# Kernel tuning notes

Measured on AMD Instinct MI355X. Metric: run time of the kernel, lower is better.

## Reference

```python
import jax, jax.numpy as jnp
import numpy as np
import math

T_SCALE = 99
FEAT_DIM = 400
BATCH = 2
C = 256
NH = 8
NS = 32
NSPB = 3
RATIO = 0.5
LOCAL_STEP = 33


def build_sample_mask(T=T_SCALE, ns=NS, nspb=NSPB, ratio=RATIO):
    # Vectorized port of _get_interp1d_mask. Flat layout: [time, (bin, start, end)].
    N = ns * nspb
    e_idx, s_idx = np.meshgrid(np.arange(T), np.arange(T), indexing='ij')
    valid = s_idx < e_idx
    starts_i = s_idx[valid].astype(np.int64)
    ends_i = e_idx[valid].astype(np.int64)
    starts = starts_i.astype(np.float64)
    ends = ends_i.astype(np.float64)
    center = ends - starts + 1.0
    xmin = starts - center * ratio
    plen = (ends + center * ratio) - xmin
    S = xmin[:, None] + (plen / (N - 1.0))[:, None] * np.arange(N)[None, :]  # [P, N]
    down = np.trunc(S).astype(np.int64)  # matches int(math.modf(s)[1]) (trunc toward 0)
    dec = S - down                       # can be negative when s < 0, as in the original
    up = np.ceil(S).astype(np.int64)
    bin_col = (np.arange(N) // nspb)[None, :] * (T * T) + (starts_i * T + ends_i)[:, None]
    M = np.zeros(T * ns * T * T, np.float64)
    vd = (down >= 0) & (down <= T - 1)
    np.add.at(M, (down * (ns * T * T) + bin_col)[vd], ((1.0 - dec) / nspb)[vd])
    vu = (up >= 0) & (up <= T - 1)
    np.add.at(M, (up * (ns * T * T) + bin_col)[vu], (dec / nspb)[vu])
    return M.reshape(T, ns * T * T).astype(np.float32)


def pos_ebb(scale, size):
    pos = jnp.arange(scale, dtype=jnp.float32)[:, None]
    div = jnp.exp(jnp.arange(0, size, 2, dtype=jnp.float32) * (-math.log(10000.0) / size))
    ang = pos * div
    # interleave sin (even) / cos (odd)
    return jnp.stack([jnp.sin(ang), jnp.cos(ang)], axis=-1).reshape(scale, size)


def layer_norm(x, g, b, eps=1e-5):
    mu = jnp.mean(x, -1, keepdims=True)
    var = jnp.mean((x - mu) ** 2, -1, keepdims=True)
    return (x - mu) * jax.lax.rsqrt(var + eps) * g + b


def mha(x, w_qkv, b_qkv, w_o, b_o, nh=NH):
    t, b, c = x.shape
    hd = c // nh
    q, k, v = jnp.split(x @ w_qkv.T + b_qkv, 3, axis=-1)
    q = q.reshape(t, b, nh, hd)
    k = k.reshape(t, b, nh, hd)
    v = v.reshape(t, b, nh, hd)
    att = jnp.einsum('qbhd,kbhd->bhqk', q, k) / math.sqrt(hd)
    att = jax.nn.softmax(att, axis=-1)
    o = jnp.einsum('bhqk,kbhd->qbhd', att, v).reshape(t, b, c)
    return o @ w_o.T + b_o


def encoder(x, p):
    # PyTorch post-norm TransformerEncoder (eval mode, dropout off) + final LayerNorm
    (qkv_w, qkv_b, o_w, o_b, l1_w, l1_b, l2_w, l2_b, n1_g, n1_b, n2_g, n2_b, nf_g, nf_b) = p
    for i in range(qkv_w.shape[0]):
        a = mha(x, qkv_w[i], qkv_b[i], o_w[i], o_b[i])
        x = layer_norm(x + a, n1_g[i], n1_b[i])
        f = jax.nn.relu(x @ l1_w[i].T + l1_b[i]) @ l2_w[i].T + l2_b[i]
        x = layer_norm(x + f, n2_g[i], n2_b[i])
    return layer_norm(x, nf_g, nf_b)


def conv1d(x, w, b, pad, groups=1):
    y = jax.lax.conv_general_dilated(x, w, (1,), [(pad, pad)],
                                     dimension_numbers=('NCH', 'OIH', 'NCH'),
                                     feature_group_count=groups)
    return y + b[None, :, None]


def conv2d(x, w, b, pad):
    y = jax.lax.conv_general_dilated(x, w, (1, 1), [(pad, pad), (pad, pad)],
                                     dimension_numbers=('NCHW', 'OIHW', 'NCHW'))
    return y + b[None, :, None, None]


def conv3d(x, w, b, stride):
    y = jax.lax.conv_general_dilated(x, w, stride, [(0, 0)] * 3,
                                     dimension_numbers=('NCDHW', 'OIDHW', 'NCDHW'))
    return y + b[None, :, None, None, None]


def _forward(x, cb_w, cb_b, tg_qkv_w, tg_qkv_b, tg_o_w, tg_o_b, tg_l1_w, tg_l1_b, tg_l2_w, tg_l2_b, tg_n1_g, tg_n1_b, tg_n2_g, tg_n2_b, tg_nf_g, tg_nf_b, tl_qkv_w, tl_qkv_b, tl_o_w, tl_o_b, tl_l1_w, tl_l1_b, tl_l2_w, tl_l2_b, tl_n1_g, tl_n1_b, tl_n2_g, tl_n2_b, tl_nf_g, tl_nf_b, s1_w, s1_b, s2_w, s2_b, c3_w, c3_b, p1_w, p1_b, p2_w, p2_b, p3_w, p3_b, sample_mask):
    B, _, T = x.shape
    base = jax.nn.relu(conv1d(x, cb_w, cb_b, pad=1, groups=4))  # [B,C,T]
    # local transformer on LOCAL_STEP-strided windows
    group = T // LOCAL_STEP
    tl_p = (tl_qkv_w, tl_qkv_b, tl_o_w, tl_o_b, tl_l1_w, tl_l1_b, tl_l2_w, tl_l2_b, tl_n1_g, tl_n1_b, tl_n2_g, tl_n2_b, tl_nf_g, tl_nf_b)
    feat = base.reshape(B, C, LOCAL_STEP, group).transpose(2, 3, 0, 1).reshape(LOCAL_STEP, B * group, C)
    feat = encoder(feat + pos_ebb(LOCAL_STEP, C)[:, None, :], tl_p)
    local = feat.reshape(LOCAL_STEP * group, B, C).transpose(1, 2, 0)  # [B,C,T]
    # global bidirectional transformer (shared weights, flipped second pass)
    tg_p = (tg_qkv_w, tg_qkv_b, tg_o_w, tg_o_b, tg_l1_w, tg_l1_b, tg_l2_w, tg_l2_b, tg_n1_g, tg_n1_b, tg_n2_g, tg_n2_b, tg_nf_g, tg_nf_b)
    g = base.transpose(2, 0, 1)  # [T,B,C]
    pe = pos_ebb(T, C)[:, None, :]
    f1 = encoder(g + pe, tg_p)
    f2 = encoder(g[::-1] + pe, tg_p)
    base2 = local + (f1 + f2[::-1]).transpose(1, 2, 0)  # [B,C,T]
    s = jax.nn.relu(conv1d(base2, s1_w, s1_b, pad=1, groups=4))
    start1 = jax.nn.sigmoid(conv1d(s, s2_w, s2_b, pad=0))[:, 0, :]  # [B,T]
    # boundary-matching layer: dense matmul against precomputed interp mask
    bm = jnp.matmul(base2, sample_mask).reshape(B, C, NS, T, T)
    p = jax.nn.relu(conv3d(bm, c3_w, c3_b, (NS, 1, 1)))[:, :, 0]  # [B,C,T,T]
    p = jax.nn.relu(conv2d(p, p1_w, p1_b, pad=1))
    p = jax.nn.relu(conv2d(p, p2_w, p2_b, pad=1))
    cm = jax.nn.sigmoid(conv2d(p, p3_w, p3_b, pad=0))  # [B,2,T,T]
    return cm, start1


def setup_inputs() -> dict:
    key = jax.random.key(0)
    ks = iter(jax.random.split(key, 80))
    def rnd(shape):
        return 0.02 * jax.random.normal(next(ks), shape, dtype=jnp.float32)
    inp = {'x': jax.random.normal(next(ks), (BATCH, FEAT_DIM, T_SCALE), dtype=jnp.float32)}
    inp['cb_w'] = rnd((C, FEAT_DIM // 4, 3)); inp['cb_b'] = jnp.zeros((C,), jnp.float32)
    for pre, n in (('tg', 6), ('tl', 3)):
        inp[pre + '_qkv_w'] = rnd((n, 3 * C, C)); inp[pre + '_qkv_b'] = jnp.zeros((n, 3 * C), jnp.float32)
        inp[pre + '_o_w'] = rnd((n, C, C)); inp[pre + '_o_b'] = jnp.zeros((n, C), jnp.float32)
        inp[pre + '_l1_w'] = rnd((n, 1024, C)); inp[pre + '_l1_b'] = jnp.zeros((n, 1024), jnp.float32)
        inp[pre + '_l2_w'] = rnd((n, C, 1024)); inp[pre + '_l2_b'] = jnp.zeros((n, C), jnp.float32)
        inp[pre + '_n1_g'] = jnp.ones((n, C), jnp.float32); inp[pre + '_n1_b'] = jnp.zeros((n, C), jnp.float32)
        inp[pre + '_n2_g'] = jnp.ones((n, C), jnp.float32); inp[pre + '_n2_b'] = jnp.zeros((n, C), jnp.float32)
        inp[pre + '_nf_g'] = jnp.ones((C,), jnp.float32); inp[pre + '_nf_b'] = jnp.zeros((C,), jnp.float32)
    inp['s1_w'] = rnd((C, C // 4, 3)); inp['s1_b'] = jnp.zeros((C,), jnp.float32)
    inp['s2_w'] = rnd((1, C, 1)); inp['s2_b'] = jnp.zeros((1,), jnp.float32)
    inp['c3_w'] = rnd((C, C, NS, 1, 1)); inp['c3_b'] = jnp.zeros((C,), jnp.float32)
    inp['p1_w'] = rnd((C, C, 3, 3)); inp['p1_b'] = jnp.zeros((C,), jnp.float32)
    inp['p2_w'] = rnd((C, C, 3, 3)); inp['p2_b'] = jnp.zeros((C,), jnp.float32)
    inp['p3_w'] = rnd((2, C, 1, 1)); inp['p3_b'] = jnp.zeros((2,), jnp.float32)
    inp['sample_mask'] = jnp.asarray(build_sample_mask())  # [T, NS*T*T], exact BMN interp mask
    return inp


def reference(x, cb_w, cb_b, tg_qkv_w, tg_qkv_b, tg_o_w, tg_o_b, tg_l1_w, tg_l1_b, tg_l2_w, tg_l2_b, tg_n1_g, tg_n1_b, tg_n2_g, tg_n2_b, tg_nf_g, tg_nf_b, tl_qkv_w, tl_qkv_b, tl_o_w, tl_o_b, tl_l1_w, tl_l1_b, tl_l2_w, tl_l2_b, tl_n1_g, tl_n1_b, tl_n2_g, tl_n2_b, tl_nf_g, tl_nf_b, s1_w, s1_b, s2_w, s2_b, c3_w, c3_b, p1_w, p1_b, p2_w, p2_b, p3_w, p3_b, sample_mask):
    return _forward(x, cb_w, cb_b, tg_qkv_w, tg_qkv_b, tg_o_w, tg_o_b, tg_l1_w, tg_l1_b, tg_l2_w, tg_l2_b, tg_n1_g, tg_n1_b, tg_n2_g, tg_n2_b, tg_nf_g, tg_nf_b, tl_qkv_w, tl_qkv_b, tl_o_w, tl_o_b, tl_l1_w, tl_l1_b, tl_l2_w, tl_l2_b, tl_n1_g, tl_n1_b, tl_n2_g, tl_n2_b, tl_nf_g, tl_nf_b, s1_w, s1_b, s2_w, s2_b, c3_w, c3_b, p1_w, p1_b, p2_w, p2_b, p3_w, p3_b, sample_mask)
```

## Files before the change

### kernel.cpp

```cpp
#include <hip/hip_runtime.h>
#include <math.h>

#define T99   99
#define CC    256
#define NHH   8
#define FEAT  400
#define NS_   32
#define LSTEP 33

typedef __attribute__((ext_vector_type(8))) short s8v;
typedef __attribute__((ext_vector_type(4))) float f4v;

__device__ __forceinline__ void mfma_bf16(f4v& d, s8v a, s8v b) {
  asm("v_mfma_f32_16x16x32_bf16 %0, %1, %2, %0" : "+v"(d) : "v"(a), "v"(b));
}

__device__ __forceinline__ unsigned short f2bf(float f) {
  union { float f; unsigned u; } x; x.f = f;
  unsigned r = x.u + 0x7FFFu + ((x.u >> 16) & 1u);
  return (unsigned short)(r >> 16);
}
__device__ __forceinline__ float bf2f(unsigned short h) {
  union { unsigned u; float f; } x; x.u = ((unsigned)h) << 16;
  return x.f;
}
__device__ __forceinline__ float blo(unsigned u) { union { unsigned x; float f; } c; c.x = u << 16; return c.f; }
__device__ __forceinline__ float bhi(unsigned u) { union { unsigned x; float f; } c; c.x = u & 0xffff0000u; return c.f; }

__device__ __forceinline__ float pe_val(int pos, int c) {
  int i = c >> 1;
  float freq = expf((float)(2 * i) * (-0.03597789207803197f));
  float ang = (float)pos * freq;
  return (c & 1) ? cosf(ang) : sinf(ang);
}

__global__ __launch_bounds__(128) void k_convbase(const float* __restrict__ x,
                                                  const float* __restrict__ w,
                                                  const float* __restrict__ bias,
                                                  float* __restrict__ base) {
  int b = blockIdx.x >> 8, co = blockIdx.x & 255, t = threadIdx.x;
  if (t >= T99) return;
  int g = co >> 6;
  float acc = bias[co];
  const float* xp = x + (size_t)(b * FEAT + g * 100) * T99;
  const float* wp = w + (size_t)co * 300;
  for (int ic = 0; ic < 100; ++ic) {
    float x0 = (t > 0)  ? xp[ic * T99 + t - 1] : 0.f;
    float x1 = xp[ic * T99 + t];
    float x2 = (t < 98) ? xp[ic * T99 + t + 1] : 0.f;
    acc += wp[ic * 3] * x0 + wp[ic * 3 + 1] * x1 + wp[ic * 3 + 2] * x2;
  }
  base[(size_t)(b * CC + co) * T99 + t] = fmaxf(acc, 0.f);
}

__global__ __launch_bounds__(256) void k_convW(const float* __restrict__ qkv, const float* __restrict__ o,
                                               const float* __restrict__ l1, const float* __restrict__ l2,
                                               int L, unsigned short* __restrict__ dst) {
  int total = L * 786432;
  for (int idx = blockIdx.x * 256 + threadIdx.x; idx < total; idx += gridDim.x * 256) {
    int l = idx / 786432, r = idx % 786432;
    float v;
    if (r < 196608)      v = qkv[(size_t)l * 196608 + r];
    else if (r < 262144) v = o[(size_t)l * 65536 + (r - 196608)];
    else if (r < 524288) v = l1[(size_t)l * 262144 + (r - 262144)];
    else                 v = l2[(size_t)l * 262144 + (r - 524288)];
    dst[idx] = f2bf(v);
  }
}

__global__ __launch_bounds__(256) void k_build_xg(const float* __restrict__ base, float* __restrict__ xg,
                                                  unsigned short* __restrict__ xgb) {
  int idx = blockIdx.x * 256 + threadIdx.x;
  int t = idx >> 10, r = idx & 1023, b4 = r >> 8, c = r & 255;
  float v = (b4 < 2) ? base[(size_t)(b4 * CC + c) * T99 + t]
                     : base[(size_t)((b4 - 2) * CC + c) * T99 + (98 - t)];
  v += pe_val(t, c);
  xg[idx] = v; xgb[idx] = f2bf(v);
}

__global__ __launch_bounds__(256) void k_build_xl(const float* __restrict__ base, float* __restrict__ xl,
                                                  unsigned short* __restrict__ xlb) {
  int idx = blockIdx.x * 256 + threadIdx.x;
  int ls = idx / 1536, r = idx % 1536, j = r >> 8, c = r & 255;
  int g = j >> 1, b = j & 1, t = ls * 3 + g;
  float v = base[(size_t)(b * CC + c) * T99 + t] + pe_val(ls, c);
  xl[idx] = v; xlb[idx] = f2bf(v);
}

struct GJ {
  const unsigned short* Ab;
  const unsigned short* W;
  const float* bias;
  const float* R;
  float* Yf;
  unsigned short* Yb;
  int M, N, K, flags;
};

__device__ void g_body(const GJ& j, int m0, int n0) {
  __shared__ __align__(16) unsigned short Al[64][264];
  __shared__ __align__(16) unsigned short Bl[64][264];
  int tid = threadIdx.x, lane = tid & 63, w = tid >> 6, wm = w >> 1, wn = w & 1;
  f4v acc[2][2];
#pragma unroll
  for (int mt = 0; mt < 2; ++mt)
#pragma unroll
    for (int nt = 0; nt < 2; ++nt) acc[mt][nt] = (f4v){0.f, 0.f, 0.f, 0.f};

  for (int kc0 = 0; kc0 < j.K; kc0 += 256) {
#pragma unroll
    for (int it = 0; it < 8; ++it) {
      int idx = it * 256 + tid, row = idx >> 5, seg = (idx & 31) << 3;
      s8v av = {0, 0, 0, 0, 0, 0, 0, 0};
      if (m0 + row < j.M) av = *(const s8v*)&j.Ab[(size_t)(m0 + row) * j.K + kc0 + seg];
      *(s8v*)&Al[row][seg] = av;
      *(s8v*)&Bl[row][seg] = *(const s8v*)&j.W[(size_t)(n0 + row) * j.K + kc0 + seg];
    }
    __syncthreads();
#pragma unroll
    for (int kst = 0; kst < 8; ++kst) {
      int kcol = kst * 32 + (lane >> 4) * 8;
      s8v af[2], bf[2];
#pragma unroll
      for (int mt = 0; mt < 2; ++mt)
        af[mt] = *(const s8v*)&Al[wm * 32 + mt * 16 + (lane & 15)][kcol];
#pragma unroll
      for (int nt = 0; nt < 2; ++nt)
        bf[nt] = *(const s8v*)&Bl[wn * 32 + nt * 16 + (lane & 15)][kcol];
#pragma unroll
      for (int mt = 0; mt < 2; ++mt)
#pragma unroll
        for (int nt = 0; nt < 2; ++nt) mfma_bf16(acc[mt][nt], af[mt], bf[nt]);
    }
    __syncthreads();
  }
  asm volatile("s_nop 7\n\ts_nop 7\n\ts_nop 4");
#pragma unroll
  for (int mt = 0; mt < 2; ++mt) {
#pragma unroll
    for (int nt = 0; nt < 2; ++nt) {
      int col = n0 + wn * 32 + nt * 16 + (lane & 15);
      float bv = j.bias[col];
#pragma unroll
      for (int r = 0; r < 4; ++r) {
        int row = m0 + wm * 32 + mt * 16 + (lane >> 4) * 4 + r;
        if (row < j.M) {
          float v = acc[mt][nt][r] + bv;
          if (j.flags & 2) v += j.R[(size_t)row * j.N + col];
          if (j.flags & 1) v = fmaxf(v, 0.f);
          if (!(j.flags & 8)) j.Yf[(size_t)row * j.N + col] = v;
          if (j.flags & 4) j.Yb[(size_t)row * j.N + col] = f2bf(v);
        }
      }
    }
  }
}

__global__ __launch_bounds__(256) void k_g(GJ j) {
  if ((int)blockIdx.x * 64 >= j.M) return;
  g_body(j, blockIdx.x * 64, blockIdx.y * 64);
}

__global__ __launch_bounds__(256) void k_g2(GJ j0, GJ j1) {
  if (blockIdx.z == 0) {
    if ((int)blockIdx.x * 64 >= j0.M) return;
    g_body(j0, blockIdx.x * 64, blockIdx.y * 64);
  } else {
    if ((int)blockIdx.x * 64 >= j1.M) return;
    g_body(j1, blockIdx.x * 64, blockIdx.y * 64);
  }
}

__device__ __forceinline__ void attn_body(const unsigned short* __restrict__ qkv,
                                          unsigned short* __restrict__ attb,
                                          int T_, int B_, int bid) {
  __shared__ float qv[32];
  __shared__ float red[128];
  __shared__ float pv[128];
  int tid = threadIdx.x;
  int q = bid % T_;
  int h = (bid / T_) % NHH;
  int b = bid / (T_ * NHH);
  if (tid < 32) qv[tid] = bf2f(qkv[(size_t)(q * B_ + b) * 768 + h * 32 + tid]);
  __syncthreads();
  float s = -1e30f;
  if (tid < T_) {
    const unsigned short* kp = qkv + (size_t)(tid * B_ + b) * 768 + 256 + h * 32;
    float d = 0;
#pragma unroll
    for (int i = 0; i < 32; ++i) d += qv[i] * bf2f(kp[i]);
    s = d * 0.176776695296636881f;
  }
  red[tid] = s; __syncthreads();
  for (int o = 64; o > 0; o >>= 1) { if (tid < o) red[tid] = fmaxf(red[tid], red[tid + o]); __syncthreads(); }
  float mx = red[0]; __syncthreads();
  float p = (tid < T_) ? expf(s - mx) : 0.f;
  pv[tid] = p; red[tid] = p; __syncthreads();
  for (int o = 64; o > 0; o >>= 1) { if (tid < o) red[tid] += red[tid + o]; __syncthreads(); }
  float denom = red[0];
  __syncthreads();
  int d = tid & 31, part = tid >> 5;
  float o = 0.f;
  for (int k = part; k < T_; k += 4)
    o += pv[k] * bf2f(qkv[(size_t)(k * B_ + b) * 768 + 512 + h * 32 + d]);
  red[tid] = o; __syncthreads();
  if (tid < 32) {
    float t = red[tid] + red[tid + 32] + red[tid + 64] + red[tid + 96];
    attb[(size_t)(q * B_ + b) * 256 + h * 32 + tid] = f2bf(t / denom);
  }
}

__global__ __launch_bounds__(128) void k_attn(const unsigned short* __restrict__ qkv,
                                              unsigned short* __restrict__ attb, int T_, int B_) {
  attn_body(qkv, attb, T_, B_, blockIdx.x);
}

__global__ __launch_bounds__(128) void k_attn2(const unsigned short* __restrict__ qkv0,
                                               unsigned short* __restrict__ attb0, int T0, int B0,
                                               const unsigned short* __restrict__ qkv1,
                                               unsigned short* __restrict__ attb1, int T1, int B1) {
  int bid = blockIdx.x;
  if (blockIdx.z == 0) {
    if (bid >= B0 * NHH * T0) return;
    attn_body(qkv0, attb0, T0, B0, bid);
  } else {
    if (bid >= B1 * NHH * T1) return;
    attn_body(qkv1, attb1, T1, B1, bid);
  }
}

__device__ __forceinline__ void ln_body(const float* __restrict__ X, const float* __restrict__ g,
                                        const float* __restrict__ bb, float* __restrict__ Y,
                                        unsigned short* __restrict__ Yb, int tok) {
  __shared__ float rs[256], rq[256];
  int c = threadIdx.x;
  float v = X[(size_t)tok * 256 + c];
  rs[c] = v; rq[c] = v * v; __syncthreads();
  for (int o = 128; o > 0; o >>= 1) { if (c < o) { rs[c] += rs[c + o]; rq[c] += rq[c + o]; } __syncthreads(); }
  float mu = rs[0] * (1.f / 256.f);
  float var = rq[0] * (1.f / 256.f) - mu * mu;
  float r = (v - mu) * rsqrtf(var + 1e-5f) * g[c] + bb[c];
  Y[(size_t)tok * 256 + c] = r;
  if (Yb) Yb[(size_t)tok * 256 + c] = f2bf(r);
}

__global__ __launch_bounds__(256) void k_ln(const float* __restrict__ X, const float* __restrict__ g,
                                            const float* __restrict__ bb, float* __restrict__ Y,
                                            unsigned short* __restrict__ Yb) {
  ln_body(X, g, bb, Y, Yb, blockIdx.x);
}

__global__ __launch_bounds__(256) void k_ln2(const float* __restrict__ X0, const float* __restrict__ g0,
                                             const float* __restrict__ bb0, float* __restrict__ Y0,
                                             unsigned short* __restrict__ Yb0, int n0,
                                             const float* __restrict__ X1, const float* __restrict__ g1,
                                             const float* __restrict__ bb1, float* __restrict__ Y1,
                                             unsigned short* __restrict__ Yb1, int n1) {
  int tok = blockIdx.x;
  if (blockIdx.z == 0) { if (tok < n0) ln_body(X0, g0, bb0, Y0, Yb0, tok); }
  else                 { if (tok < n1) ln_body(X1, g1, bb1, Y1, Yb1, tok); }
}

__global__ __launch_bounds__(256) void k_combine(const float* __restrict__ encl, const float* __restrict__ encg,
                                                 float* __restrict__ base2) {
  int idx = blockIdx.x * 256 + threadIdx.x;
  int t = idx % T99, c = (idx / T99) & 255, b = idx / (CC * T99);
  int ls = t / 3, g = t % 3;
  float v = encl[(size_t)(ls * 6 + g * 2 + b) * 256 + c]
          + encg[(size_t)(t * 4 + b) * 256 + c]
          + encg[(size_t)((98 - t) * 4 + 2 + b) * 256 + c];
  base2[idx] = v;
}

__global__ __launch_bounds__(256) void k_sfuse(const float* __restrict__ base2, const float* __restrict__ s1w,
                                               const float* __restrict__ s1b, const float* __restrict__ s2w,
                                               const float* __restrict__ s2b, float* __restrict__ out) {
  __shared__ float rs[256];
  int b = blockIdx.x / T99, t = blockIdx.x % T99, co = threadIdx.x;
  int g = co >> 6;
  float acc = s1b[co];
  const float* xp = base2 + (size_t)(b * CC + g * 64) * T99;
  const float* wp = s1w + (size_t)co * 192;
  for (int ic = 0; ic < 64; ++ic) {
    float x0 = (t > 0)  ? xp[ic * T99 + t - 1] : 0.f;
    float x1 = xp[ic * T99 + t];
    float x2 = (t < 98) ? xp[ic * T99 + t + 1] : 0.f;
    acc += wp[ic * 3] * x0 + wp[ic * 3 + 1] * x1 + wp[ic * 3 + 2] * x2;
  }
  rs[co] = fmaxf(acc, 0.f) * s2w[co];
  __syncthreads();
  for (int o = 128; o > 0; o >>= 1) { if (co < o) rs[co] += rs[co + o]; __syncthreads(); }
  if (co == 0) out[blockIdx.x] = 1.f / (1.f + expf(-(rs[0] + s2b[0])));
}

__global__ __launch_bounds__(256) void k_w3t(const float* __restrict__ c3w, float* __restrict__ w3t) {
  int idx = blockIdx.x * 256 + threadIdx.x;
  int co = idx & 255, ci = (idx >> 8) & 255, n = idx >> 16;
  w3t[idx] = c3w[((size_t)(co << 8) + ci) * 32 + n];
}

__global__ __launch_bounds__(256) void k_G(const float* __restrict__ w3t, const float* __restrict__ base2,
                                           unsigned short* __restrict__ Gb) {
  int tc = blockIdx.x, n = blockIdx.y, b = blockIdx.z;
  int co = threadIdx.x;
  int t0 = tc * 25;
  float acc[25];
#pragma unroll
  for (int q = 0; q < 25; ++q) acc[q] = 0.f;
  const float* w = w3t + (size_t)n * 65536 + co;
  const float* bs = base2 + (size_t)b * CC * T99 + t0;
  for (int ci = 0; ci < 256; ++ci) {
    float wv = w[(size_t)ci * 256];
#pragma unroll
    for (int q = 0; q < 25; ++q) acc[q] += wv * bs[ci * T99 + q];
  }
#pragma unroll
  for (int q = 0; q < 25; ++q) {
    int t = t0 + q;
    if (t < T99) Gb[((size_t)(n * T99 + t) * 256 + co) * 2 + b] = f2bf(acc[q]);
  }
  if (tc == 0 && n == 0 && b == 0)
    ((unsigned int*)(Gb + (size_t)NS_ * T99 * 512))[co] = 0u;
}

__global__ __launch_bounds__(256) void k_ppre(const unsigned short* __restrict__ Gb,
                                              const float* __restrict__ c3b,
                                              unsigned int* __restrict__ pinb32) {
  __shared__ float w0s[96], w1s[96];
  __shared__ int   ofs[96];
  __shared__ float part[128][4];
  int e = blockIdx.x % T99, s = blockIdx.x / T99;
  int tid = threadIdx.x;
  if (s >= e) {
    if (tid < 128) {
      float z0 = fmaxf(c3b[2 * tid], 0.f), z1 = fmaxf(c3b[2 * tid + 1], 0.f);
      unsigned int zz = ((unsigned)f2bf(z1) << 16) | (unsigned)f2bf(z0);
      pinb32[((size_t)s * T99 + e) * 128 + tid] = zz;
      pinb32[((size_t)(T99 + s) * T99 + e) * 128 + tid] = zz;
    }
    return;
  }
  if (tid < 96) {
    double center = (double)(e - s + 1);
    double S = ((double)s - 0.5 * center) + ((2.0 * center - 1.0) / 95.0) * (double)tid;
    double dn = trunc(S);
    double dec = S - dn;
    int di = (int)dn;
    double uc = ceil(S);
    int ui = (int)uc;
    int n = tid / 3;
    float w0 = 0.f, w1 = 0.f;
    int r0 = 0;
    if (dn >= 0.0 && dn <= 98.0) {
      r0 = di;
      w0 = (float)((1.0 - dec) / 3.0);
      if (uc >= 0.0 && uc <= 98.0) {
        if (ui == di) w0 += (float)(dec / 3.0);
        else          w1  = (float)(dec / 3.0);
      }
    }
    w0s[tid] = w0; w1s[tid] = w1;
    ofs[tid] = (n * T99 + r0) * 1024;
  }
  __syncthreads();
  int ch = tid & 127, half = tid >> 7;
  float a00 = 0.f, a01 = 0.f, a10 = 0.f, a11 = 0.f;
  const char* basep = (const char*)Gb + ch * 8;
  int k0 = half * 48;
#pragma unroll 8
  for (int k = k0; k < k0 + 48; ++k) {
    float w0 = w0s[k], w1 = w1s[k];
    const uint2* p = (const uint2*)(basep + ofs[k]);
    uint2 u0 = p[0];
    uint2 u1 = p[128];
    a00 += w0 * blo(u0.x) + w1 * blo(u1.x);
    a01 += w0 * bhi(u0.x) + w1 * bhi(u1.x);
    a10 += w0 * blo(u0.y) + w1 * blo(u1.y);
    a11 += w0 * bhi(u0.y) + w1 * bhi(u1.y);
  }
  if (half) { part[ch][0] = a00; part[ch][1] = a01; part[ch][2] = a10; part[ch][3] = a11; }
  __syncthreads();
  if (tid < 128) {
    a00 += part[ch][0]; a01 += part[ch][1]; a10 += part[ch][2]; a11 += part[ch][3];
    float b0 = c3b[2 * tid], b1 = c3b[2 * tid + 1];
    unsigned int zb0 = ((unsigned)f2bf(fmaxf(a10 + b1, 0.f)) << 16) | (unsigned)f2bf(fmaxf(a00 + b0, 0.f));
    unsigned int zb1 = ((unsigned)f2bf(fmaxf(a11 + b1, 0.f)) << 16) | (unsigned)f2bf(fmaxf(a01 + b0, 0.f));
    pinb32[((size_t)s * T99 + e) * 128 + tid] = zb0;
    pinb32[((size_t)(T99 + s) * T99 + e) * 128 + tid] = zb1;
  }
}

__global__ __launch_bounds__(256) void k_wb2(const float* __restrict__ pw, unsigned short* __restrict__ wbf) {
  int idx = blockIdx.x * 256 + threadIdx.x;
  if (idx >= 73728) return;
  int lane = idx & 63;
  int cog  = (idx >> 6) & 15;
  int kst  = (idx >> 10) & 7;
  int tap  = idx >> 13;
  int co = cog * 16 + (lane & 15);
  int k  = kst * 32 + (lane >> 4) * 8;
  s8v v;
#pragma unroll
  for (int j = 0; j < 8; ++j)
    v[j] = (short)f2bf(pw[((size_t)co * 256 + k + j) * 9 + tap]);
  *(s8v*)&wbf[(size_t)idx * 8] = v;
}

__global__ __launch_bounds__(256) void k_cvec(const float* __restrict__ pw, const float* __restrict__ cin,
                                              const float* __restrict__ bias, int reluCin,
                                              float* __restrict__ coutF, unsigned short* __restrict__ coutB) {
  __shared__ float rs[256];
  int co = blockIdx.x, ci = threadIdx.x;
  float c = cin[ci];
  if (reluCin) c = fmaxf(c, 0.f);
  const float* wp = pw + ((size_t)co * 256 + ci) * 9;
  float wsum = 0.f;
#pragma unroll
  for (int t = 0; t < 9; ++t) wsum += wp[t];
  rs[ci] = wsum * c;
  __syncthreads();
  for (int o = 128; o > 0; o >>= 1) { if (ci < o) rs[ci] += rs[ci + o]; __syncthreads(); }
  if (ci == 0) {
    float r = fmaxf(bias[co] + rs[0], 0.f);
    coutF[co] = r;
    coutB[co] = f2bf(r);
  }
}

__device__ __forceinline__ int aoff(int s) {
  int tap = s >> 3, kst = s & 7;
  return ((tap / 3) * 10 + (tap % 3)) * 264 + kst * 32;
}
__device__ __forceinline__ void ldb4(const unsigned short* __restrict__ B0, int s, s8v* dst) {
#pragma unroll
  for (int nt = 0; nt < 4; ++nt) dst[nt] = *(const s8v*)(B0 + (size_t)s * 8192 + nt * 512);
}

__global__ __launch_bounds__(256) void k_conv3x3(const unsigned short* __restrict__ in,
                                                 const unsigned short* __restrict__ wbf,
                                                 const float* __restrict__ bias,
                                                 const unsigned short* __restrict__ cvecB,
                                                 int D, int lo, int hi,
                                                 unsigned short* __restrict__ out) {
  __shared__ __align__(16) unsigned short Ah[100 * 264];
  int b = blockIdx.z;
  int co0 = blockIdx.y * 128;
  int ti = blockIdx.x / 13, tj = blockIdx.x % 13;
  int i0 = ti * 8, j0 = tj * 8;
  int tid = threadIdx.x;

  if (i0 - 1 >= lo && i0 + 8 <= hi && j0 - 1 >= lo && j0 + 8 <= hi && i0 - 1 >= j0 + 8 + D) {
    const unsigned int* cv = (const unsigned int*)(cvecB + co0);
    unsigned int* ob = (unsigned int*)out;
#pragma unroll
    for (int r = 0; r < 16; ++r) {
      int idx = r * 256 + tid;
      int sp = idx >> 6, cp = idx & 63;
      int gi = i0 + (sp >> 3), gj = j0 + (sp & 7);
      ob[((size_t)(b * T99 + gi) * T99 + gj) * 128 + (co0 >> 1) + cp] = cv[cp];
    }
    return;
  }

#pragma unroll
  for (int it = 0; it < 13; ++it) {
    int chunk = it * 256 + tid;
    if (chunk < 3200) {
      int row = chunk >> 5;
      int cc = (chunk & 31) * 8;
      int gi = i0 + row / 10 - 1, gj = j0 + row % 10 - 1;
      s8v val = {0, 0, 0, 0, 0, 0, 0, 0};
      if (gi >= 0 && gi < T99 && gj >= 0 && gj < T99)
        val = *(const s8v*)&in[((size_t)(b * T99 + gi) * T99 + gj) * 256 + cc];
      *(s8v*)&Ah[row * 264 + cc] = val;
    }
  }
  __syncthreads();

  int lane = tid & 63, w = tid >> 6, wm = w >> 1, wn = w & 1;
  int l15 = lane & 15, lk = lane >> 4;
  int spL0 = wm * 32 + l15, spL1 = spL0 + 16;
  int hr0 = (spL0 >> 3) * 10 + (spL0 & 7);
  int hr1 = (spL1 >> 3) * 10 + (spL1 & 7);
  const unsigned short* A0 = &Ah[hr0 * 264 + lk * 8];
  const unsigned short* A1 = &Ah[hr1 * 264 + lk * 8];
  int cogbase = blockIdx.y * 8 + wn * 4;
  const unsigned short* B0 = wbf + (size_t)cogbase * 512 + (size_t)lane * 8;

  f4v acc[2][4];
#pragma unroll
  for (int mt = 0; mt < 2; ++mt)
#pragma unroll
    for (int nt = 0; nt < 4; ++nt) acc[mt][nt] = (f4v){0.f, 0.f, 0.f, 0.f};

  s8v a0c, a1c, a0n, a1n;
  s8v bq[3][4];
  a0c = *(const s8v*)(A0 + aoff(0));
  a1c = *(const s8v*)(A1 + aoff(0));
  a0n = a0c; a1n = a1c;
  ldb4(B0, 0, bq[0]);
  ldb4(B0, 1, bq[1]);
#pragma unroll
  for (int s = 0; s < 72; ++s) {
    if (s + 2 < 72) ldb4(B0, s + 2, bq[(s + 2) % 3]);
    if (s + 1 < 72) {
      a0n = *(const s8v*)(A0 + aoff(s + 1));
      a1n = *(const s8v*)(A1 + aoff(s + 1));
    }
#pragma unroll
    for (int nt = 0; nt < 4; ++nt) {
      mfma_bf16(acc[0][nt], a0c, bq[s % 3][nt]);
      mfma_bf16(acc[1][nt], a1c, bq[s % 3][nt]);
    }
    a0c = a0n; a1c = a1n;
  }

  asm volatile("s_nop 7\n\ts_nop 7\n\ts_nop 4");
#pragma unroll
  for (int mt = 0; mt < 2; ++mt) {
#pragma unroll
    for (int nt = 0; nt < 4; ++nt) {
      int co = co0 + wn * 64 + nt * 16 + l15;
      float bv = bias[co];
#pragma unroll
      for (int r = 0; r < 4; ++r) {
        int sp = wm * 32 + mt * 16 + lk * 4 + r;
        int gi = i0 + (sp >> 3), gj = j0 + (sp & 7);
        if (gi < T99 && gj < T99) {
          float v = fmaxf(acc[mt][nt][r] + bv, 0.f);
          out[((size_t)(b * T99 + gi) * T99 + gj) * 256 + co] = f2bf(v);
        }
      }
    }
  }
}

__global__ __launch_bounds__(256) void k_p3(const unsigned short* __restrict__ p2o,
                                            const float* __restrict__ w, const float* __restrict__ bias,
                                            float* __restrict__ cm) {
  int idx = blockIdx.x * 256 + threadIdx.x;
  if (idx >= 2 * T99 * T99) return;
  int j = idx % T99, i = (idx / T99) % T99, b = idx / (T99 * T99);
  float a0 = bias[0], a1 = bias[1];
  const unsigned short* row = p2o + ((size_t)(b * T99 + i) * T99 + j) * 256;
  for (int c8 = 0; c8 < 256; c8 += 8) {
    s8v v = *(const s8v*)&row[c8];
#pragma unroll
    for (int q = 0; q < 8; ++q) {
      float x = bf2f((unsigned short)v[q]);
      a0 += w[c8 + q] * x;
      a1 += w[256 + c8 + q] * x;
    }
  }
  size_t base = (size_t)b * 2 * T99 * T99 + (size_t)i * T99 + j;
  cm[base] = 1.f / (1.f + expf(-a0));
  cm[base + T99 * T99] = 1.f / (1.f + expf(-a1));
}

struct EncW {
  const float *qkvw, *qkvb, *ow, *ob, *l1w, *l1b, *l2w, *l2b, *n1g, *n1b, *n2g, *n2b, *nfg, *nfb;
};
struct EncBufs {
  float* x; unsigned short* xb;
  float* yb;
  unsigned short *qkvb, *attb, *hb;
  int M;
};

static GJ jqkv(const EncW& W, const unsigned short* Wb, int l, const EncBufs& B) {
  GJ j = {}; j.Ab = B.xb; j.W = Wb + (size_t)l * 786432;
  j.bias = W.qkvb + (size_t)l * 768; j.Yb = B.qkvb; j.flags = 4 | 8;
  j.M = B.M; j.N = 768; j.K = 256; return j;
}
static GJ jproj(const EncW& W, const unsigned short* Wb, int l, const EncBufs& B) {
  GJ j = {}; j.Ab = B.attb; j.W = Wb + (size_t)l * 786432 + 196608;
  j.bias = W.ob + (size_t)l * 256; j.R = B.x; j.Yf = B.yb; j.flags = 2;
  j.M = B.M; j.N = 256; j.K = 256; return j;
}
static GJ jffn1(const EncW& W, const unsigned short* Wb, int l, const EncBufs& B) {
  GJ j = {}; j.Ab = B.xb; j.W = Wb + (size_t)l * 786432 + 262144;
  j.bias = W.l1b + (size_t)l * 1024; j.Yb = B.hb; j.flags = 1 | 4 | 8;
  j.M = B.M; j.N = 1024; j.K = 256; return j;
}
static GJ jffn2(const EncW& W, const unsigned short* Wb, int l, const EncBufs& B) {
  GJ j = {}; j.Ab = B.hb; j.W = Wb + (size_t)l * 786432 + 524288;
  j.bias = W.l2b + (size_t)l * 256; j.R = B.x; j.Yf = B.yb; j.flags = 2;
  j.M = B.M; j.N = 256; j.K = 1024; return j;
}

extern "C" void kernel_launch(void* const* d_in, const int* in_sizes, int n_in,
                              void* d_out, int out_size, void* d_ws, size_t ws_size,
                              hipStream_t stream) {
  (void)in_sizes; (void)n_in; (void)out_size; (void)ws_size;
  const float* x    = (const float*)d_in[0];
  const float* cbw  = (const float*)d_in[1];
  const float* cbb  = (const float*)d_in[2];
  EncW tg = {(const float*)d_in[3],  (const float*)d_in[4],  (const float*)d_in[5],  (const float*)d_in[6],
             (const float*)d_in[7],  (const float*)d_in[8],  (const float*)d_in[9],  (const float*)d_in[10],
             (const float*)d_in[11], (const float*)d_in[12], (const float*)d_in[13], (const float*)d_in[14],
             (const float*)d_in[15], (const float*)d_in[16]};
  EncW tl = {(const float*)d_in[17], (const float*)d_in[18], (const float*)d_in[19], (const float*)d_in[20],
             (const float*)d_in[21], (const float*)d_in[22], (const float*)d_in[23], (const float*)d_in[24],
             (const float*)d_in[25], (const float*)d_in[26], (const float*)d_in[27], (const float*)d_in[28],
             (const float*)d_in[29], (const float*)d_in[30]};
  const float* s1w = (const float*)d_in[31];
  const float* s1b = (const float*)d_in[32];
  const float* s2w = (const float*)d_in[33];
  const float* s2b = (const float*)d_in[34];
  const float* c3w = (const float*)d_in[35];
  const float* c3b = (const float*)d_in[36];
  const float* p1w = (const float*)d_in[37];
  const float* p1b = (const float*)d_in[38];
  const float* p2w = (const float*)d_in[39];
  const float* p2b = (const float*)d_in[40];
  const float* p3w = (const float*)d_in[41];
  const float* p3b = (const float*)d_in[42];

  float* outp = (float*)d_out;

  char* wp = (char*)d_ws;
  auto alloc = [&](size_t bytes) -> void* {
    void* p = (void*)wp;
    wp += (bytes + 255) & ~(size_t)255;
    return p;
  };
  float* base  = (float*)alloc(sizeof(float) * 2 * CC * T99);
  const int ML = 198, MG = 396;
  EncBufs BG, BL;
  BG.M = MG; BL.M = ML;
  BG.x  = (float*)alloc(sizeof(float) * MG * 256);
  BL.x  = (float*)alloc(sizeof(float) * ML * 256);
  BG.xb = (unsigned short*)alloc(sizeof(short) * MG * 256);
  BL.xb = (unsigned short*)alloc(sizeof(short) * ML * 256);
  BG.yb = (float*)alloc(sizeof(float) * MG * 256);
  BL.yb = (float*)alloc(sizeof(float) * ML * 256);
  BG.qkvb = (unsigned short*)alloc(sizeof(short) * MG * 768);
  BL.qkvb = (unsigned short*)alloc(sizeof(short) * ML * 768);
  BG.attb = (unsigned short*)alloc(sizeof(short) * MG * 256);
  BL.attb = (unsigned short*)alloc(sizeof(short) * ML * 256);
  BG.hb = (unsigned short*)alloc(sizeof(short) * MG * 1024);
  BL.hb = (unsigned short*)alloc(sizeof(short) * ML * 1024);
  float* encg  = (float*)alloc(sizeof(float) * MG * 256);
  float* encl  = (float*)alloc(sizeof(float) * ML * 256);
  float* base2 = (float*)alloc(sizeof(float) * 2 * CC * T99);
  float* w3t   = (float*)alloc(sizeof(float) * 32 * 256 * 256);
  unsigned short* Gb = (unsigned short*)alloc(sizeof(short) * (2 * NS_ * T99 * 256 + 512));
  unsigned short* pinb = (unsigned short*)alloc(sizeof(short) * 2 * T99 * T99 * 256);
  unsigned short* p1o  = (unsigned short*)alloc(sizeof(short) * 2 * T99 * T99 * 256);
  unsigned short* p2o  = (unsigned short*)alloc(sizeof(short) * 2 * T99 * T99 * 256);
  unsigned short* wb2a = (unsigned short*)alloc(sizeof(short) * 9 * 256 * 256);
  unsigned short* wb2b = (unsigned short*)alloc(sizeof(short) * 9 * 256 * 256);
  unsigned short* wtgb = (unsigned short*)alloc(sizeof(short) * 6 * 786432);
  unsigned short* wtlb = (unsigned short*)alloc(sizeof(short) * 3 * 786432);
  float* c1F = (float*)alloc(sizeof(float) * 256);
  unsigned short* c1B = (unsigned short*)alloc(sizeof(short) * 256);
  float* c2F = (float*)alloc(sizeof(float) * 256);
  unsigned short* c2B = (unsigned short*)alloc(sizeof(short) * 256);

  k_convW<<<dim3(4096), dim3(256), 0, stream>>>(tg.qkvw, tg.ow, tg.l1w, tg.l2w, 6, wtgb);
  k_convW<<<dim3(2048), dim3(256), 0, stream>>>(tl.qkvw, tl.ow, tl.l1w, tl.l2w, 3, wtlb);
  k_w3t<<<dim3(8192), dim3(256), 0, stream>>>(c3w, w3t);
  k_wb2<<<dim3(288), dim3(256), 0, stream>>>(p1w, wb2a);
  k_wb2<<<dim3(288), dim3(256), 0, stream>>>(p2w, wb2b);
  k_cvec<<<dim3(256), dim3(256), 0, stream>>>(p1w, c3b, p1b, 1, c1F, c1B);
  k_cvec<<<dim3(256), dim3(256), 0, stream>>>(p2w, c1F, p2b, 0, c2F, c2B);
  k_convbase<<<dim3(512), dim3(128), 0, stream>>>(x, cbw, cbb, base);
  k_build_xl<<<dim3(198), dim3(256), 0, stream>>>(base, BL.x, BL.xb);
  k_build_xg<<<dim3(396), dim3(256), 0, stream>>>(base, BG.x, BG.xb);

  const int mgG = 7;
  for (int l = 0; l < 3; ++l) {
    k_g2<<<dim3(mgG, 12, 2), dim3(256), 0, stream>>>(jqkv(tl, wtlb, l, BL), jqkv(tg, wtgb, l, BG));
    k_attn2<<<dim3(4 * NHH * T99, 1, 2), dim3(128), 0, stream>>>(BL.qkvb, BL.attb, LSTEP, 6,
                                                                 BG.qkvb, BG.attb, T99, 4);
    k_g2<<<dim3(mgG, 4, 2), dim3(256), 0, stream>>>(jproj(tl, wtlb, l, BL), jproj(tg, wtgb, l, BG));
    k_ln2<<<dim3(MG, 1, 2), dim3(256), 0, stream>>>(BL.yb, tl.n1g + l * 256, tl.n1b + l * 256, BL.x, BL.xb, ML,
                                                    BG.yb, tg.n1g + l * 256, tg.n1b + l * 256, BG.x, BG.xb, MG);
    k_g2<<<dim3(mgG, 16, 2), dim3(256), 0, stream>>>(jffn1(tl, wtlb, l, BL), jffn1(tg, wtgb, l, BG));
    k_g2<<<dim3(mgG, 4, 2), dim3(256), 0, stream>>>(jffn2(tl, wtlb, l, BL), jffn2(tg, wtgb, l, BG));
    k_ln2<<<dim3(MG, 1, 2), dim3(256), 0, stream>>>(BL.yb, tl.n2g + l * 256, tl.n2b + l * 256, BL.x, BL.xb, ML,
                                                    BG.yb, tg.n2g + l * 256, tg.n2b + l * 256, BG.x, BG.xb, MG);
  }
  for (int l = 3; l < 6; ++l) {
    k_g<<<dim3(mgG, 12), dim3(256), 0, stream>>>(jqkv(tg, wtgb, l, BG));
    k_attn<<<dim3(4 * NHH * T99), dim3(128), 0, stream>>>(BG.qkvb, BG.attb, T99, 4);
    k_g<<<dim3(mgG, 4), dim3(256), 0, stream>>>(jproj(tg, wtgb, l, BG));
    k_ln<<<dim3(MG), dim3(256), 0, stream>>>(BG.yb, tg.n1g + l * 256, tg.n1b + l * 256, BG.x, BG.xb);
    k_g<<<dim3(mgG, 16), dim3(256), 0, stream>>>(jffn1(tg, wtgb, l, BG));
    k_g<<<dim3(mgG, 4), dim3(256), 0, stream>>>(jffn2(tg, wtgb, l, BG));
    k_ln<<<dim3(MG), dim3(256), 0, stream>>>(BG.yb, tg.n2g + l * 256, tg.n2b + l * 256, BG.x, BG.xb);
  }
  k_ln2<<<dim3(MG, 1, 2), dim3(256), 0, stream>>>(BL.x, tl.nfg, tl.nfb, encl, nullptr, ML,
                                                  BG.x, tg.nfg, tg.nfb, encg, nullptr, MG);
  k_combine<<<dim3(198), dim3(256), 0, stream>>>(encl, encg, base2);
  k_sfuse<<<dim3(198), dim3(256), 0, stream>>>(base2, s1w, s1b, s2w, s2b, outp + 2 * 2 * T99 * T99);
  k_G<<<dim3(4, 32, 2), dim3(256), 0, stream>>>(w3t, base2, Gb);
  k_ppre<<<dim3(T99 * T99), dim3(256), 0, stream>>>(Gb, c3b, (unsigned int*)pinb);
  k_conv3x3<<<dim3(169, 2, 2), dim3(256), 0, stream>>>(pinb, wb2a, p1b, c1B, 0, 0, 98, p1o);
  k_conv3x3<<<dim3(169, 2, 2), dim3(256), 0, stream>>>(p1o, wb2b, p2b, c2B, 2, 1, 97, p2o);
  k_p3<<<dim3(77), dim3(256), 0, stream>>>(p2o, p3w, p3b, outp);
}
```

Before: 688.1 us.

## Move G projection to bf16 MFMA and shrink GEMM LDS tiles to K=32

The fp32 scalar k_G kernel becomes an MFMA-based bf16 GEMM (k_Gm). It uses a transposed bf16 copy of base2 produced in k_combine and a bf16 transposed weight w3tb. The shared transformer GEMM body also now stages 32-wide K slices instead of 256-wide ones. This shrinks LDS use, which should allow higher occupancy, but adds more barriers per K step. Rounding the G inputs to bf16 lowers precision.

```diff
diff --git a/kernel.cpp b/kernel.cpp
--- a/kernel.cpp
+++ b/kernel.cpp
@@ -98,40 +98,35 @@
 };
 
 __device__ void g_body(const GJ& j, int m0, int n0) {
-  __shared__ __align__(16) unsigned short Al[64][264];
-  __shared__ __align__(16) unsigned short Bl[64][264];
-  int tid = threadIdx.x, lane = tid & 63, w = tid >> 6, wm = w >> 1, wn = w & 1;
+  __shared__ __align__(16) unsigned short Al[64][40];
+  __shared__ __align__(16) unsigned short Bl[64][40];
+  int tid = threadIdx.x;
+  int lane = tid & 63, w = tid >> 6, wm = w >> 1, wn = w & 1;
+  int sp = tid >> 2, kc = (tid & 3) << 3;
   f4v acc[2][2];
 #pragma unroll
   for (int mt = 0; mt < 2; ++mt)
 #pragma unroll
     for (int nt = 0; nt < 2; ++nt) acc[mt][nt] = (f4v){0.f, 0.f, 0.f, 0.f};
 
-  for (int kc0 = 0; kc0 < j.K; kc0 += 256) {
-#pragma unroll
-    for (int it = 0; it < 8; ++it) {
-      int idx = it * 256 + tid, row = idx >> 5, seg = (idx & 31) << 3;
-      s8v av = {0, 0, 0, 0, 0, 0, 0, 0};
-      if (m0 + row < j.M) av = *(const s8v*)&j.Ab[(size_t)(m0 + row) * j.K + kc0 + seg];
-      *(s8v*)&Al[row][seg] = av;
-      *(s8v*)&Bl[row][seg] = *(const s8v*)&j.W[(size_t)(n0 + row) * j.K + kc0 + seg];
-    }
+  for (int k0 = 0; k0 < j.K; k0 += 32) {
+    s8v av = {0, 0, 0, 0, 0, 0, 0, 0};
+    int row = m0 + sp;
+    if (row < j.M) av = *(const s8v*)&j.Ab[(size_t)row * j.K + k0 + kc];
+    *(s8v*)&Al[sp][kc] = av;
+    *(s8v*)&Bl[sp][kc] = *(const s8v*)&j.W[(size_t)(n0 + sp) * j.K + k0 + kc];
     __syncthreads();
-#pragma unroll
-    for (int kst = 0; kst < 8; ++kst) {
-      int kcol = kst * 32 + (lane >> 4) * 8;
-      s8v af[2], bf[2];
-#pragma unroll
-      for (int mt = 0; mt < 2; ++mt)
-        af[mt] = *(const s8v*)&Al[wm * 32 + mt * 16 + (lane & 15)][kcol];
-#pragma unroll
-      for (int nt = 0; nt < 2; ++nt)
-        bf[nt] = *(const s8v*)&Bl[wn * 32 + nt * 16 + (lane & 15)][kcol];
-#pragma unroll
-      for (int mt = 0; mt < 2; ++mt)
-#pragma unroll
-        for (int nt = 0; nt < 2; ++nt) mfma_bf16(acc[mt][nt], af[mt], bf[nt]);
-    }
+    s8v af[2], bf[2];
+#pragma unroll
+    for (int mt = 0; mt < 2; ++mt)
+      af[mt] = *(const s8v*)&Al[wm * 32 + mt * 16 + (lane & 15)][(lane >> 4) * 8];
+#pragma unroll
+    for (int nt = 0; nt < 2; ++nt)
+      bf[nt] = *(const s8v*)&Bl[wn * 32 + nt * 16 + (lane & 15)][(lane >> 4) * 8];
+#pragma unroll
+    for (int mt = 0; mt < 2; ++mt)
+#pragma unroll
+      for (int nt = 0; nt < 2; ++nt) mfma_bf16(acc[mt][nt], af[mt], bf[nt]);
     __syncthreads();
   }
   asm volatile("s_nop 7\n\ts_nop 7\n\ts_nop 4");
@@ -262,7 +257,7 @@
 }
 
 __global__ __launch_bounds__(256) void k_combine(const float* __restrict__ encl, const float* __restrict__ encg,
-                                                 float* __restrict__ base2) {
+                                                 float* __restrict__ base2, unsigned short* __restrict__ b2t) {
   int idx = blockIdx.x * 256 + threadIdx.x;
   int t = idx % T99, c = (idx / T99) & 255, b = idx / (CC * T99);
   int ls = t / 3, g = t % 3;
@@ -270,6 +265,7 @@
           + encg[(size_t)(t * 4 + b) * 256 + c]
           + encg[(size_t)((98 - t) * 4 + 2 + b) * 256 + c];
   base2[idx] = v;
+  b2t[((size_t)(b * T99) + t) * 256 + c] = f2bf(v);
 }
 
 __global__ __launch_bounds__(256) void k_sfuse(const float* __restrict__ base2, const float* __restrict__ s1w,
@@ -293,34 +289,66 @@
   if (co == 0) out[blockIdx.x] = 1.f / (1.f + expf(-(rs[0] + s2b[0])));
 }
 
-__global__ __launch_bounds__(256) void k_w3t(const float* __restrict__ c3w, float* __restrict__ w3t) {
+__global__ __launch_bounds__(256) void k_w3tb(const float* __restrict__ c3w, unsigned short* __restrict__ w3tb) {
   int idx = blockIdx.x * 256 + threadIdx.x;
-  int co = idx & 255, ci = (idx >> 8) & 255, n = idx >> 16;
-  w3t[idx] = c3w[((size_t)(co << 8) + ci) * 32 + n];
-}
-
-__global__ __launch_bounds__(256) void k_G(const float* __restrict__ w3t, const float* __restrict__ base2,
-                                           unsigned short* __restrict__ Gb) {
-  int tc = blockIdx.x, n = blockIdx.y, b = blockIdx.z;
-  int co = threadIdx.x;
-  int t0 = tc * 25;
-  float acc[25];
-#pragma unroll
-  for (int q = 0; q < 25; ++q) acc[q] = 0.f;
-  const float* w = w3t + (size_t)n * 65536 + co;
-  const float* bs = base2 + (size_t)b * CC * T99 + t0;
-  for (int ci = 0; ci < 256; ++ci) {
-    float wv = w[(size_t)ci * 256];
-#pragma unroll
-    for (int q = 0; q < 25; ++q) acc[q] += wv * bs[ci * T99 + q];
-  }
-#pragma unroll
-  for (int q = 0; q < 25; ++q) {
-    int t = t0 + q;
-    if (t < T99) Gb[((size_t)(n * T99 + t) * 256 + co) * 2 + b] = f2bf(acc[q]);
-  }
-  if (tc == 0 && n == 0 && b == 0)
-    ((unsigned int*)(Gb + (size_t)NS_ * T99 * 512))[co] = 0u;
+  int ci = idx & 255, co = (idx >> 8) & 255, n = idx >> 16;
+  w3tb[idx] = f2bf(c3w[((size_t)(co << 8) + ci) * 32 + n]);
+}
+
+__global__ __launch_bounds__(256) void k_Gm(const unsigned short* __restrict__ b2t,
+                                            const unsigned short* __restrict__ w3tb,
+                                            unsigned short* __restrict__ Gb) {
+  __shared__ __align__(16) unsigned short Al[64][40];
+  __shared__ __align__(16) unsigned short Bl[64][40];
+  int nb = blockIdx.z, n = nb >> 1, b = nb & 1;
+  int m0 = blockIdx.x * 64, n0 = blockIdx.y * 64;
+  int tid = threadIdx.x;
+  if (blockIdx.x == 0 && blockIdx.y == 0 && nb == 0)
+    ((unsigned int*)(Gb + (size_t)NS_ * T99 * 512))[tid] = 0u;
+  const unsigned short* A = b2t + (size_t)b * T99 * 256;
+  const unsigned short* W = w3tb + (size_t)n * 65536;
+  int lane = tid & 63, w = tid >> 6, wm = w >> 1, wn = w & 1;
+  int sp = tid >> 2, kc = (tid & 3) << 3;
+  f4v acc[2][2];
+#pragma unroll
+  for (int mt = 0; mt < 2; ++mt)
+#pragma unroll
+    for (int nt = 0; nt < 2; ++nt) acc[mt][nt] = (f4v){0.f, 0.f, 0.f, 0.f};
+#pragma unroll
+  for (int k0 = 0; k0 < 256; k0 += 32) {
+    s8v av = {0, 0, 0, 0, 0, 0, 0, 0};
+    int row = m0 + sp;
+    if (row < T99) av = *(const s8v*)&A[(size_t)row * 256 + k0 + kc];
+    *(s8v*)&Al[sp][kc] = av;
+    *(s8v*)&Bl[sp][kc] = *(const s8v*)&W[(size_t)(n0 + sp) * 256 + k0 + kc];
+    __syncthreads();
+    s8v af[2], bf[2];
+#pragma unroll
+    for (int mt = 0; mt < 2; ++mt)
+      af[mt] = *(const s8v*)&Al[wm * 32 + mt * 16 + (lane & 15)][(lane >> 4) * 8];
+#pragma unroll
+    for (int nt = 0; nt < 2; ++nt)
+      bf[nt] = *(const s8v*)&Bl[wn * 32 + nt * 16 + (lane & 15)][(lane >> 4) * 8];
+#pragma unroll
+    for (int mt = 0; mt < 2; ++mt)
+#pragma unroll
+      for (int nt = 0; nt < 2; ++nt) mfma_bf16(acc[mt][nt], af[mt], bf[nt]);
+    __syncthreads();
+  }
+  asm volatile("s_nop 7\n\ts_nop 7\n\ts_nop 4");
+#pragma unroll
+  for (int mt = 0; mt < 2; ++mt) {
+#pragma unroll
+    for (int nt = 0; nt < 2; ++nt) {
+      int co = n0 + wn * 32 + nt * 16 + (lane & 15);
+#pragma unroll
+      for (int r = 0; r < 4; ++r) {
+        int t = m0 + wm * 32 + mt * 16 + (lane >> 4) * 4 + r;
+        if (t < T99)
+          Gb[((size_t)(n * T99 + t) * 256 + co) * 2 + b] = f2bf(acc[mt][nt][r]);
+      }
+    }
+  }
 }
 
 __global__ __launch_bounds__(256) void k_ppre(const unsigned short* __restrict__ Gb,
@@ -643,7 +671,8 @@
   float* encg  = (float*)alloc(sizeof(float) * MG * 256);
   float* encl  = (float*)alloc(sizeof(float) * ML * 256);
   float* base2 = (float*)alloc(sizeof(float) * 2 * CC * T99);
-  float* w3t   = (float*)alloc(sizeof(float) * 32 * 256 * 256);
+  unsigned short* b2t = (unsigned short*)alloc(sizeof(short) * 2 * T99 * 256);
+  unsigned short* w3tb = (unsigned short*)alloc(sizeof(short) * 32 * 256 * 256);
   unsigned short* Gb = (unsigned short*)alloc(sizeof(short) * (2 * NS_ * T99 * 256 + 512));
   unsigned short* pinb = (unsigned short*)alloc(sizeof(short) * 2 * T99 * T99 * 256);
   unsigned short* p1o  = (unsigned short*)alloc(sizeof(short) * 2 * T99 * T99 * 256);
@@ -659,7 +688,7 @@
 
   k_convW<<<dim3(4096), dim3(256), 0, stream>>>(tg.qkvw, tg.ow, tg.l1w, tg.l2w, 6, wtgb);
   k_convW<<<dim3(2048), dim3(256), 0, stream>>>(tl.qkvw, tl.ow, tl.l1w, tl.l2w, 3, wtlb);
-  k_w3t<<<dim3(8192), dim3(256), 0, stream>>>(c3w, w3t);
+  k_w3tb<<<dim3(8192), dim3(256), 0, stream>>>(c3w, w3tb);
   k_wb2<<<dim3(288), dim3(256), 0, stream>>>(p1w, wb2a);
   k_wb2<<<dim3(288), dim3(256), 0, stream>>>(p2w, wb2b);
   k_cvec<<<dim3(256), dim3(256), 0, stream>>>(p1w, c3b, p1b, 1, c1F, c1B);
@@ -692,9 +721,9 @@
   }
   k_ln2<<<dim3(MG, 1, 2), dim3(256), 0, stream>>>(BL.x, tl.nfg, tl.nfb, encl, nullptr, ML,
                                                   BG.x, tg.nfg, tg.nfb, encg, nullptr, MG);
-  k_combine<<<dim3(198), dim3(256), 0, stream>>>(encl, encg, base2);
+  k_combine<<<dim3(198), dim3(256), 0, stream>>>(encl, encg, base2, b2t);
   k_sfuse<<<dim3(198), dim3(256), 0, stream>>>(base2, s1w, s1b, s2w, s2b, outp + 2 * 2 * T99 * T99);
-  k_G<<<dim3(4, 32, 2), dim3(256), 0, stream>>>(w3t, base2, Gb);
+  k_Gm<<<dim3(2, 4, 64), dim3(256), 0, stream>>>(b2t, w3tb, Gb);
   k_ppre<<<dim3(T99 * T99), dim3(256), 0, stream>>>(Gb, c3b, (unsigned int*)pinb);
   k_conv3x3<<<dim3(169, 2, 2), dim3(256), 0, stream>>>(pinb, wb2a, p1b, c1B, 0, 0, 98, p1o);
   k_conv3x3<<<dim3(169, 2, 2), dim3(256), 0, stream>>>(p1o, wb2b, p2b, c2B, 2, 1, 97, p2o);
```

Measured after the change: 635.4 us. 7.7% less time.
